# Kernel optimization log

Hardware: AMD Instinct MI355X
Metric: run time of the kernel (lower is better)

The kernel has to match this reference:

```python
import jax, jax.numpy as jnp
import numpy as np

# config (matches init_kwargs)
D_MODEL = 2048
EXPAND = 2
HEADDIM = 64
D_STATE = 128
D_CONV = 4
NGROUPS = 1  # reference implemented for ngroups == 1
CHUNK = 256
EPS = 1e-5
D_INNER = EXPAND * D_MODEL            # 4096
NHEADS = D_INNER // HEADDIM           # 64
CONV_DIM = D_INNER + 2 * NGROUPS * D_STATE   # 4352
D_IN_PROJ = 2 * D_INNER + 2 * NGROUPS * D_STATE + NHEADS  # 8512
BATCH, SEQLEN = 2, 2048


def segsum(a):
    # a: [..., q] log-decays -> [..., q, q] with entry (i,j) = sum_{j<k<=i} a_k, -inf above diag
    T = a.shape[-1]
    cs = jnp.cumsum(a, axis=-1)
    d = cs[..., :, None] - cs[..., None, :]
    mask = jnp.tril(jnp.ones((T, T), dtype=bool))
    return jnp.where(mask, d, -jnp.inf)


def setup_inputs() -> dict:
    key = jax.random.key(0)
    ks = jax.random.split(key, 8)
    u = jax.random.normal(ks[0], (BATCH, SEQLEN, D_MODEL), jnp.float32)
    in_proj_w = jax.random.normal(ks[1], (D_IN_PROJ, D_MODEL), jnp.float32) / np.sqrt(D_MODEL).astype(np.float32)
    conv_w = jax.random.normal(ks[2], (CONV_DIM, D_CONV), jnp.float32) / np.sqrt(D_CONV).astype(np.float32)
    conv_b = jnp.zeros((CONV_DIM,), jnp.float32)
    # dt_bias init as in module: inv-softplus of dt ~ LogUniform(1e-3, 1e-1)
    dt0 = jnp.exp(jax.random.uniform(ks[3], (NHEADS,), jnp.float32)
                  * (np.log(0.1) - np.log(0.001)) + np.log(0.001))
    dt0 = jnp.clip(dt0, 1e-4, None)
    dt_bias = dt0 + jnp.log(-jnp.expm1(-dt0))
    A_log = jnp.log(jax.random.uniform(ks[4], (NHEADS,), jnp.float32, minval=1.0, maxval=16.0))
    D = jnp.ones((NHEADS,), jnp.float32)
    norm_w = jnp.ones((D_INNER,), jnp.float32)
    out_proj_w = jax.random.normal(ks[5], (D_MODEL, D_INNER), jnp.float32) / np.sqrt(D_INNER).astype(np.float32)
    return dict(u=u, in_proj_w=in_proj_w, conv_w=conv_w, conv_b=conv_b,
                dt_bias=dt_bias, A_log=A_log, D=D, norm_w=norm_w, out_proj_w=out_proj_w)


def reference(u, in_proj_w, conv_w, conv_b, dt_bias, A_log, D, norm_w, out_proj_w):
    b, l, _ = u.shape
    # in_proj -> [z | xBC | dt]  (d_mlp == 0 for this config)
    zxbcdt = jnp.einsum('bld,ed->ble', u, in_proj_w)
    z = zxbcdt[..., :D_INNER]
    xBC = zxbcdt[..., D_INNER:D_INNER + CONV_DIM]
    dt = zxbcdt[..., D_INNER + CONV_DIM:]                      # [b,l,h]

    # causal depthwise conv1d + SiLU (kernel D_CONV, left padding)
    xp = jnp.pad(xBC, ((0, 0), (D_CONV - 1, 0), (0, 0)))
    conv = conv_b
    for k in range(D_CONV):
        conv = conv + xp[:, k:k + l, :] * conv_w[:, k]
    xBC = jax.nn.silu(conv)

    x = xBC[..., :D_INNER]
    Bm = xBC[..., D_INNER:D_INNER + D_STATE]                   # [b,l,n] (ngroups=1)
    Cm = xBC[..., D_INNER + D_STATE:]                          # [b,l,n]

    dtv = jax.nn.softplus(dt + dt_bias)                        # [b,l,h]
    A = -jnp.exp(A_log)                                        # [h]
    xh = x.reshape(b, l, NHEADS, HEADDIM)

    # ---- chunked SSD scan (mamba_chunk_scan_combined) ----
    c = l // CHUNK
    xc = (xh * dtv[..., None]).reshape(b, c, CHUNK, NHEADS, HEADDIM)   # dt-scaled inputs
    Ac = (dtv * A).reshape(b, c, CHUNK, NHEADS).transpose(0, 3, 1, 2)  # [b,h,c,q] log decays
    Bc = Bm.reshape(b, c, CHUNK, D_STATE)
    Cc = Cm.reshape(b, c, CHUNK, D_STATE)

    Acum = jnp.cumsum(Ac, axis=-1)                              # [b,h,c,q]
    Lmat = jnp.exp(segsum(Ac))                                  # [b,h,c,q,q] causal decay matrix
    # intra-chunk (diagonal block) contribution
    Y_diag = jnp.einsum('bcqn,bcsn,bhcqs,bcshp->bcqhp', Cc, Bc, Lmat, xc)
    # per-chunk end states
    decay_states = jnp.exp(Acum[..., -1:] - Acum)               # [b,h,c,q]
    states = jnp.einsum('bcsn,bhcs,bcshp->bchpn', Bc, decay_states, xc)
    chunk_decay = jnp.exp(Acum[..., -1])                        # [b,h,c]

    def step(S, inp):
        st, dec = inp                                           # [b,h,p,n], [b,h]
        return dec[..., None, None] * S + st, S

    S0 = jnp.zeros((b, NHEADS, HEADDIM, D_STATE), xc.dtype)
    _, prev = jax.lax.scan(step, S0,
                           (states.transpose(1, 0, 2, 3, 4), chunk_decay.transpose(2, 0, 1)))
    prev = prev.transpose(1, 0, 2, 3, 4)                        # [b,c,h,p,n] states entering each chunk
    # inter-chunk contribution
    Y_off = jnp.einsum('bcqn,bchpn,bhcq->bcqhp', Cc, prev, jnp.exp(Acum))

    y = (Y_diag + Y_off).reshape(b, l, NHEADS, HEADDIM)
    y = y + D[:, None] * xh                                     # skip connection D*x
    # gate (applied inside kernel via z=...), then gated RMSNorm (z-less here), then out_proj
    y = y.reshape(b, l, D_INNER) * jax.nn.silu(z)
    y = y * jax.lax.rsqrt(jnp.mean(jnp.square(y), axis=-1, keepdims=True) + EPS) * norm_w
    return jnp.einsum('bld,ed->ble', y, out_proj_w)
```

## Files before the change

### kernel.cpp

```cpp
#include <hip/hip_runtime.h>
#include <cstddef>
#include <cstdint>

#define BATCH   2
#define SEQLEN  2048
#define DMODEL  2048
#define DINNER  4096
#define NHEADS  64
#define HEADDIM 64
#define DSTATE  128
#define DCONV   4
#define CHUNKSZ 256
#define NCHUNK  (SEQLEN / CHUNKSZ)
#define CONVDIM (DINNER + 2 * DSTATE)
#define DINPROJ (2 * DINNER + 2 * DSTATE + NHEADS)
#define BL      (BATCH * SEQLEN)
#define EPSV    1e-5f

typedef __attribute__((ext_vector_type(8))) short short8v;
typedef __attribute__((ext_vector_type(4))) float floatx4;

__device__ __forceinline__ float sigmoidf_(float x) { return 1.f / (1.f + expf(-x)); }

__device__ __forceinline__ unsigned short f2bf(float x) {
  uint32_t u = __float_as_uint(x);
  uint32_t r = (u + 0x7FFFu + ((u >> 16) & 1u)) >> 16;
  return (unsigned short)r;
}
__device__ __forceinline__ float bf2f(unsigned short h) {
  return __uint_as_float(((uint32_t)h) << 16);
}

__device__ __forceinline__ void gload16(const void* g, void* l) {
  __builtin_amdgcn_global_load_lds((const __attribute__((address_space(1))) void*)g,
                                   (__attribute__((address_space(3))) void*)l, 16, 0, 0);
}

__global__ __launch_bounds__(256) void split4_kernel(const float* __restrict__ x,
                                                     unsigned short* __restrict__ hi,
                                                     unsigned short* __restrict__ lo,
                                                     int n4) {
  int i = blockIdx.x * 256 + threadIdx.x;
  if (i >= n4) return;
  float4 v = ((const float4*)x)[i];
  ushort4 hv, lv;
  hv.x = f2bf(v.x); lv.x = f2bf(v.x - bf2f(hv.x));
  hv.y = f2bf(v.y); lv.y = f2bf(v.y - bf2f(hv.y));
  hv.z = f2bf(v.z); lv.z = f2bf(v.z - bf2f(hv.z));
  hv.w = f2bf(v.w); lv.w = f2bf(v.w - bf2f(hv.w));
  ((ushort4*)hi)[i] = hv;
  ((ushort4*)lo)[i] = lv;
}

template <int EPI>
__global__ __launch_bounds__(256) void gemm3bf(const unsigned short* __restrict__ Ah,
                                               const unsigned short* __restrict__ Al, int lda,
                                               const unsigned short* __restrict__ Bh,
                                               const unsigned short* __restrict__ Bl, int ldb,
                                               int M, int N, int K,
                                               float* __restrict__ o0, float* __restrict__ o1,
                                               float* __restrict__ o2) {
  __shared__ __align__(16) unsigned short lds[4][4][128][8];
  const int tid = threadIdx.x;
  const int lane = tid & 63;
  const int w = tid >> 6, wm = w >> 1, wn = w & 1;
  const int bm = blockIdx.y * 128, bn = blockIdx.x * 128;
  const int r16 = lane & 15, kg = lane >> 4;
  floatx4 acc[4][4] = {};

  for (int k0 = 0; k0 < K; k0 += 32) {
#pragma unroll
    for (int arr = 0; arr < 4; ++arr) {
      const unsigned short* src = (arr == 0) ? Ah : (arr == 1) ? Al : (arr == 2) ? Bh : Bl;
      const int ld = (arr < 2) ? lda : ldb;
#pragma unroll
      for (int t = 0; t < 2; ++t) {
        int ubase = t * 256 + w * 64;
        int u = ubase + lane;
        int g = u >> 7, m = u & 127;
        int row;
        if (arr < 2) row = bm + m;
        else { row = bn + m; if (row >= N) row = N - 1; }
        const unsigned short* gp = src + (size_t)row * ld + k0 + g * 8;
        gload16(gp, (void*)(&lds[arr][0][0][0] + (size_t)ubase * 8));
      }
    }
    __syncthreads();

    short8v bhf[4], blf[4];
#pragma unroll
    for (int j = 0; j < 4; ++j) {
      int n_in = wn * 64 + j * 16 + r16;
      bhf[j] = *(const short8v*)&lds[2][kg][n_in][0];
      blf[j] = *(const short8v*)&lds[3][kg][n_in][0];
    }
#pragma unroll
    for (int i = 0; i < 4; ++i) {
      int m_in = wm * 64 + i * 16 + r16;
      short8v ah = *(const short8v*)&lds[0][kg][m_in][0];
      short8v al = *(const short8v*)&lds[1][kg][m_in][0];
#pragma unroll
      for (int j = 0; j < 4; ++j) {
        acc[i][j] = __builtin_amdgcn_mfma_f32_16x16x32_bf16(ah, bhf[j], acc[i][j], 0, 0, 0);
        acc[i][j] = __builtin_amdgcn_mfma_f32_16x16x32_bf16(ah, blf[j], acc[i][j], 0, 0, 0);
        acc[i][j] = __builtin_amdgcn_mfma_f32_16x16x32_bf16(al, bhf[j], acc[i][j], 0, 0, 0);
      }
    }
    __syncthreads();
  }

#pragma unroll
  for (int i = 0; i < 4; ++i) {
#pragma unroll
    for (int j = 0; j < 4; ++j) {
      int n = bn + wn * 64 + j * 16 + r16;
#pragma unroll
      for (int r = 0; r < 4; ++r) {
        int m = bm + wm * 64 + i * 16 + kg * 4 + r;
        float v = acc[i][j][r];
        if (EPI == 0) {
          o0[(size_t)m * N + n] = v;
        } else {
          if (n < DINNER) o0[(size_t)m * DINNER + n] = v;
          else if (n < DINNER + CONVDIM) o1[(size_t)m * CONVDIM + (n - DINNER)] = v;
          else if (n < DINPROJ) o2[(size_t)m * NHEADS + (n - DINNER - CONVDIM)] = v;
        }
      }
    }
  }
}

__global__ __launch_bounds__(256) void conv_silu_split(const float* __restrict__ xbc,
                                                       const float* __restrict__ cw,
                                                       const float* __restrict__ cb,
                                                       float* __restrict__ xb,
                                                       float* __restrict__ bbuf,
                                                       float* __restrict__ cbuf) {
  int idx = blockIdx.x * 256 + threadIdx.x;
  if (idx >= BL * CONVDIM) return;
  int ch = idx % CONVDIM;
  int bl = idx / CONVDIM;
  int l = bl & (SEQLEN - 1);
  int b = bl / SEQLEN;
  float acc = cb[ch];
#pragma unroll
  for (int k = 0; k < DCONV; ++k) {
    int ls = l - (DCONV - 1) + k;
    if (ls >= 0)
      acc = fmaf(xbc[((size_t)(b * SEQLEN + ls)) * CONVDIM + ch], cw[ch * DCONV + k], acc);
  }
  float s = acc * sigmoidf_(acc);
  if (ch < DINNER)
    xb[(size_t)bl * DINNER + ch] = s;
  else if (ch < DINNER + DSTATE)
    bbuf[(size_t)bl * DSTATE + (ch - DINNER)] = s;
  else
    cbuf[(size_t)bl * DSTATE + (ch - DINNER - DSTATE)] = s;
}

__global__ __launch_bounds__(256) void dt_kernel(const float* __restrict__ dtraw,
                                                 const float* __restrict__ dt_bias,
                                                 const float* __restrict__ A_log,
                                                 float* __restrict__ dtv,
                                                 float* dAb) {
  int idx = blockIdx.x * 256 + threadIdx.x;
  if (idx >= BL * NHEADS) return;
  int h = idx & (NHEADS - 1);
  float dtr = dtraw[idx] + dt_bias[h];
  float v = (dtr > 20.f) ? dtr : log1pf(expf(dtr));
  dtv[idx] = v;
  dAb[idx] = -expf(A_log[h]) * v;
}

__global__ __launch_bounds__(256) void cumsum_kernel(const float* __restrict__ dAb,
                                                     float* __restrict__ acum,
                                                     float* __restrict__ cdec) {
  const int bch = blockIdx.x;
  const int h = bch & (NHEADS - 1);
  const int bc = bch >> 6;
  const int b = bc >> 3, c = bc & (NCHUNK - 1);
  const int s = threadIdx.x;
  __shared__ float buf[CHUNKSZ];
  buf[s] = dAb[((size_t)(b * SEQLEN) + c * CHUNKSZ + s) * NHEADS + h];
  __syncthreads();
  for (int off = 1; off < CHUNKSZ; off <<= 1) {
    float t = (s >= off) ? buf[s - off] : 0.f;
    __syncthreads();
    buf[s] += t;
    __syncthreads();
  }
  float r = buf[s];
  acum[(size_t)bch * CHUNKSZ + s] = r;
  if (s == CHUNKSZ - 1) cdec[bch] = expf(r);
}

__global__ __launch_bounds__(256) void states_kernel(const float* __restrict__ xb,
                                                     const float* __restrict__ bbuf,
                                                     const float* __restrict__ dtv,
                                                     const float* __restrict__ acum,
                                                     float* __restrict__ states) {
  const int bch = blockIdx.x;
  const int h = bch & (NHEADS - 1);
  const int bc = bch >> 6;
  const int b = bc >> 3, c = bc & (NCHUNK - 1);
  const float* ac = acum + (size_t)bch * CHUNKSZ;
  const float clast = ac[CHUNKSZ - 1];
  __shared__ float xs[32][65];
  __shared__ float bs[32][129];
  __shared__ float wsh[32];
  const int tid = threadIdx.x;
  const int tp = tid >> 4, tn = tid & 15;
  float acc[4][8] = {};
  for (int s0 = 0; s0 < CHUNKSZ; s0 += 32) {
    if (tid < 32) {
      int s = s0 + tid;
      wsh[tid] = expf(clast - ac[s]) *
                 dtv[((size_t)(b * SEQLEN) + c * CHUNKSZ + s) * NHEADS + h];
    }
    __syncthreads();
    for (int e = tid; e < 32 * 64; e += 256) {
      int s = e >> 6, pp = e & 63;
      xs[s][pp] = xb[((size_t)(b * SEQLEN) + c * CHUNKSZ + s0 + s) * DINNER + h * HEADDIM + pp] * wsh[s];
    }
    for (int e = tid; e < 32 * 128; e += 256) {
      int s = e >> 7, n = e & 127;
      bs[s][n] = bbuf[((size_t)(b * SEQLEN) + c * CHUNKSZ + s0 + s) * DSTATE + n];
    }
    __syncthreads();
#pragma unroll 8
    for (int s = 0; s < 32; ++s) {
      float a[4], bv[8];
#pragma unroll
      for (int i = 0; i < 4; ++i) a[i] = xs[s][tp * 4 + i];
#pragma unroll
      for (int j = 0; j < 8; ++j) bv[j] = bs[s][tn * 8 + j];
#pragma unroll
      for (int i = 0; i < 4; ++i)
#pragma unroll
        for (int j = 0; j < 8; ++j)
          acc[i][j] = fmaf(a[i], bv[j], acc[i][j]);
    }
    __syncthreads();
  }
#pragma unroll
  for (int i = 0; i < 4; ++i)
#pragma unroll
    for (int j = 0; j < 8; ++j)
      states[((size_t)bch * HEADDIM + tp * 4 + i) * DSTATE + tn * 8 + j] = acc[i][j];
}

__global__ __launch_bounds__(256) void scan_kernel(float* __restrict__ states,
                                                   const float* __restrict__ cdec) {
  int idx = blockIdx.x * 256 + threadIdx.x;
  const int pn = idx & (HEADDIM * DSTATE - 1);
  const int bh = idx >> 13;
  const int h = bh & (NHEADS - 1), b = bh >> 6;
  float S = 0.f;
  for (int c = 0; c < NCHUNK; ++c) {
    int bch = (b * NCHUNK + c) * NHEADS + h;
    size_t off = (size_t)bch * (HEADDIM * DSTATE) + pn;
    float st = states[off];
    states[off] = S;
    S = fmaf(cdec[bch], S, st);
  }
}

__global__ __launch_bounds__(256) void cb_kernel(const float* __restrict__ cbuf,
                                                 const float* __restrict__ bbuf,
                                                 float* __restrict__ g0) {
  const int qb = blockIdx.x >> 2, sb = blockIdx.x & 3;
  if (sb > qb) return;
  const int bc = blockIdx.y;
  const int tid = threadIdx.x;
  __shared__ float As[16][65];
  __shared__ float Bs[16][65];
  const int lr = tid >> 2, lk = (tid & 3) << 2;
  const int tx = tid & 15, ty = tid >> 4;
  float acc[4][4] = {};
  const float* Arow = cbuf + ((size_t)bc * CHUNKSZ + qb * 64) * DSTATE;
  const float* Brow = bbuf + ((size_t)bc * CHUNKSZ + sb * 64) * DSTATE;
  for (int k0 = 0; k0 < DSTATE; k0 += 16) {
    float4 av = *(const float4*)(Arow + (size_t)lr * DSTATE + k0 + lk);
    float4 bv = *(const float4*)(Brow + (size_t)lr * DSTATE + k0 + lk);
    As[lk + 0][lr] = av.x; As[lk + 1][lr] = av.y; As[lk + 2][lr] = av.z; As[lk + 3][lr] = av.w;
    Bs[lk + 0][lr] = bv.x; Bs[lk + 1][lr] = bv.y; Bs[lk + 2][lr] = bv.z; Bs[lk + 3][lr] = bv.w;
    __syncthreads();
#pragma unroll
    for (int kk = 0; kk < 16; ++kk) {
      float a[4], bv2[4];
#pragma unroll
      for (int i = 0; i < 4; ++i) a[i] = As[kk][ty * 4 + i];
#pragma unroll
      for (int j = 0; j < 4; ++j) bv2[j] = Bs[kk][tx * 4 + j];
#pragma unroll
      for (int i = 0; i < 4; ++i)
#pragma unroll
        for (int j = 0; j < 4; ++j)
          acc[i][j] = fmaf(a[i], bv2[j], acc[i][j]);
    }
    __syncthreads();
  }
#pragma unroll
  for (int i = 0; i < 4; ++i)
#pragma unroll
    for (int j = 0; j < 4; ++j)
      g0[((size_t)bc * CHUNKSZ + qb * 64 + ty * 4 + i) * CHUNKSZ + sb * 64 + tx * 4 + j] = acc[i][j];
}

__global__ __launch_bounds__(256) void y_kernel(const float* __restrict__ xb,
                                                const float* __restrict__ cbuf,
                                                const float* __restrict__ g0,
                                                const float* __restrict__ acum,
                                                const float* __restrict__ dtv,
                                                const float* __restrict__ prevb,
                                                const float* __restrict__ Dvec,
                                                float* __restrict__ yb) {
  const int qb = blockIdx.x & 3;
  const int h = (blockIdx.x >> 2) & (NHEADS - 1);
  const int bc = blockIdx.x >> 8;
  const int b = bc >> 3, c = bc & (NCHUNK - 1);
  const int tid = threadIdx.x;
  const int tq = tid >> 4, tp = tid & 15;
  const float* ac = acum + ((size_t)bc * NHEADS + h) * CHUNKSZ;
  __shared__ float gs[64][33];
  __shared__ float xs[32][65];
  __shared__ float ps[64][33];
  const int qbase = qb * 64;
  float acc[4][4] = {};
  for (int s0 = 0; s0 < qbase + 64; s0 += 32) {
    for (int e = tid; e < 64 * 32; e += 256) {
      int q = e >> 5, s = e & 31;
      int gq = qbase + q, gsd = s0 + s;
      float v = 0.f;
      if (gsd <= gq) {
        float lw = expf(ac[gq] - ac[gsd]);
        float dv = dtv[((size_t)(b * SEQLEN) + c * CHUNKSZ + gsd) * NHEADS + h];
        v = g0[((size_t)bc * CHUNKSZ + gq) * CHUNKSZ + gsd] * lw * dv;
      }
      gs[q][s] = v;
    }
    for (int e = tid; e < 32 * 64; e += 256) {
      int s = e >> 6, pp = e & 63;
      xs[s][pp] = xb[((size_t)(b * SEQLEN) + c * CHUNKSZ + s0 + s) * DINNER + h * HEADDIM + pp];
    }
    __syncthreads();
#pragma unroll 8
    for (int s = 0; s < 32; ++s) {
      float a[4], xv[4];
#pragma unroll
      for (int i = 0; i < 4; ++i) a[i] = gs[tq * 4 + i][s];
#pragma unroll
      for (int j = 0; j < 4; ++j) xv[j] = xs[s][tp * 4 + j];
#pragma unroll
      for (int i = 0; i < 4; ++i)
#pragma unroll
        for (int j = 0; j < 4; ++j)
          acc[i][j] = fmaf(a[i], xv[j], acc[i][j]);
    }
    __syncthreads();
  }
  float acc2[4][4] = {};
  for (int n0 = 0; n0 < DSTATE; n0 += 32) {
    for (int e = tid; e < 64 * 32; e += 256) {
      int q = e >> 5, n = e & 31;
      gs[q][n] = cbuf[((size_t)(b * SEQLEN) + c * CHUNKSZ + qbase + q) * DSTATE + n0 + n];
    }
    for (int e = tid; e < 64 * 32; e += 256) {
      int pp = e >> 5, n = e & 31;
      ps[pp][n] = prevb[(((size_t)bc * NHEADS + h) * HEADDIM + pp) * DSTATE + n0 + n];
    }
    __syncthreads();
#pragma unroll 8
    for (int n = 0; n < 32; ++n) {
      float a[4], pv[4];
#pragma unroll
      for (int i = 0; i < 4; ++i) a[i] = gs[tq * 4 + i][n];
#pragma unroll
      for (int j = 0; j < 4; ++j) pv[j] = ps[tp * 4 + j][n];
#pragma unroll
      for (int i = 0; i < 4; ++i)
#pragma unroll
        for (int j = 0; j < 4; ++j)
          acc2[i][j] = fmaf(a[i], pv[j], acc2[i][j]);
    }
    __syncthreads();
  }
  const float dh = Dvec[h];
#pragma unroll
  for (int i = 0; i < 4; ++i) {
    int q = qbase + tq * 4 + i;
    float eaq = expf(ac[q]);
    size_t row = ((size_t)(b * SEQLEN) + c * CHUNKSZ + q) * DINNER + h * HEADDIM;
#pragma unroll
    for (int j = 0; j < 4; ++j) {
      int pp = tp * 4 + j;
      float xv = xb[row + pp];
      yb[row + pp] = acc[i][j] + eaq * acc2[i][j] + dh * xv;
    }
  }
}

__global__ __launch_bounds__(256) void norm_kernel(float* yb,
                                                   const float* __restrict__ zbuf,
                                                   const float* __restrict__ nw) {
  const int bl = blockIdx.x;
  float* y = yb + (size_t)bl * DINNER;
  const float* z = zbuf + (size_t)bl * DINNER;
  float vals[16];
  float ss = 0.f;
  int j = 0;
  for (int i = threadIdx.x; i < DINNER; i += 256, ++j) {
    float zz = z[i];
    float g = y[i] * zz * sigmoidf_(zz);
    vals[j] = g;
    ss = fmaf(g, g, ss);
  }
  for (int off = 32; off > 0; off >>= 1) ss += __shfl_down(ss, off, 64);
  __shared__ float red[4];
  if ((threadIdx.x & 63) == 0) red[threadIdx.x >> 6] = ss;
  __syncthreads();
  float tot = red[0] + red[1] + red[2] + red[3];
  float scale = rsqrtf(tot * (1.f / DINNER) + EPSV);
  unsigned short* yh = (unsigned short*)y;
  unsigned short* yl = yh + DINNER;
  j = 0;
  for (int i = threadIdx.x; i < DINNER; i += 256, ++j) {
    float v = vals[j] * scale * nw[i];
    unsigned short h = f2bf(v);
    yh[i] = h;
    yl[i] = f2bf(v - bf2f(h));
  }
}

extern "C" void kernel_launch(void* const* d_in, const int* in_sizes, int n_in,
                              void* d_out, int out_size, void* d_ws, size_t ws_size,
                              hipStream_t stream) {
  const float* u        = (const float*)d_in[0];
  const float* Wp       = (const float*)d_in[1];
  const float* conv_w   = (const float*)d_in[2];
  const float* conv_b   = (const float*)d_in[3];
  const float* dt_bias  = (const float*)d_in[4];
  const float* A_log    = (const float*)d_in[5];
  const float* Dvec     = (const float*)d_in[6];
  const float* norm_w   = (const float*)d_in[7];
  const float* Wo       = (const float*)d_in[8];
  float* out = (float*)d_out;

  char* p = (char*)d_ws;
  auto alloc = [&](size_t nfloats) {
    float* r = (float*)p;
    p += nfloats * sizeof(float);
    return r;
  };
  float* zbuf   = alloc((size_t)BL * DINNER);
  float* xbc    = alloc((size_t)BL * CONVDIM);
  float* dtraw  = alloc((size_t)BL * NHEADS);
  float* xb     = alloc((size_t)BL * DINNER);
  float* bbuf   = alloc((size_t)BL * DSTATE);
  float* cbuf   = alloc((size_t)BL * DSTATE);
  float* dtvb   = alloc((size_t)BL * NHEADS);
  float* acum   = alloc((size_t)BATCH * NCHUNK * NHEADS * CHUNKSZ);
  float* cdec   = alloc((size_t)BATCH * NCHUNK * NHEADS);
  float* dAb    = dtraw;
  float* states = out;
  float* g0     = xbc + (size_t)BL * DINNER;
  float* yb     = xbc;
  unsigned short* u_hi  = (unsigned short*)d_out;
  unsigned short* u_lo  = u_hi + (size_t)BL * DMODEL;
  unsigned short* wp_hi = (unsigned short*)xb;
  unsigned short* wp_lo = wp_hi + (size_t)DINPROJ * DMODEL;
  unsigned short* wo_hi = (unsigned short*)zbuf;
  unsigned short* wo_lo = wo_hi + (size_t)DMODEL * DINNER;
  unsigned short* yo_hi = (unsigned short*)xbc;
  unsigned short* yo_lo = yo_hi + DINNER;

  split4_kernel<<<(BL * DMODEL / 4 + 255) / 256, 256, 0, stream>>>(u, u_hi, u_lo, BL * DMODEL / 4);
  split4_kernel<<<(DINPROJ * DMODEL / 4 + 255) / 256, 256, 0, stream>>>(Wp, wp_hi, wp_lo,
                                                                        DINPROJ * DMODEL / 4);
  gemm3bf<1><<<dim3((DINPROJ + 127) / 128, BL / 128), 256, 0, stream>>>(
      u_hi, u_lo, DMODEL, wp_hi, wp_lo, DMODEL, BL, DINPROJ, DMODEL, zbuf, xbc, dtraw);
  conv_silu_split<<<(BL * CONVDIM + 255) / 256, 256, 0, stream>>>(xbc, conv_w, conv_b, xb, bbuf, cbuf);
  dt_kernel<<<(BL * NHEADS + 255) / 256, 256, 0, stream>>>(dtraw, dt_bias, A_log, dtvb, dAb);
  cumsum_kernel<<<BATCH * NCHUNK * NHEADS, CHUNKSZ, 0, stream>>>(dAb, acum, cdec);
  states_kernel<<<BATCH * NCHUNK * NHEADS, 256, 0, stream>>>(xb, bbuf, dtvb, acum, states);
  scan_kernel<<<(BATCH * NHEADS * HEADDIM * DSTATE) / 256, 256, 0, stream>>>(states, cdec);
  cb_kernel<<<dim3(16, BATCH * NCHUNK), 256, 0, stream>>>(cbuf, bbuf, g0);
  y_kernel<<<BATCH * NCHUNK * NHEADS * 4, 256, 0, stream>>>(xb, cbuf, g0, acum, dtvb, states, Dvec, yb);
  norm_kernel<<<BL, 256, 0, stream>>>(yb, zbuf, norm_w);
  split4_kernel<<<(DMODEL * DINNER / 4 + 255) / 256, 256, 0, stream>>>(Wo, wo_hi, wo_lo,
                                                                      DMODEL * DINNER / 4);
  gemm3bf<0><<<dim3(DMODEL / 128, BL / 128), 256, 0, stream>>>(
      yo_hi, yo_lo, 2 * DINNER, wo_hi, wo_lo, DINNER, BL, DMODEL, DINNER, out, nullptr, nullptr);
}
```

Before: 1.735 ms.

## Double-buffer LDS in split-bf16 GEMM, add grouped XCD-aware tile swizzle

Gives the 3xbf16 GEMM two LDS buffers, so the next K-slice's global-to-LDS loads are issued before the current slice's MFMAs. This cuts one barrier per iteration. The launch becomes a 1D grid remapped through an XCD-round-robin swizzle and grouped-M ordering to improve L2 reuse of the operand tiles. Output stores become nontemporal. LDS use doubles to 64KB per block, which may lower occupancy, and nontemporal stores could hurt the consumer kernels that reread these outputs.

```diff
diff --git a/kernel.cpp b/kernel.cpp
--- a/kernel.cpp
+++ b/kernel.cpp
@@ -60,45 +60,69 @@
                                                int M, int N, int K,
                                                float* __restrict__ o0, float* __restrict__ o1,
                                                float* __restrict__ o2) {
-  __shared__ __align__(16) unsigned short lds[4][4][128][8];
+  __shared__ __align__(16) unsigned short lds[2][4][4][128][8];
   const int tid = threadIdx.x;
   const int lane = tid & 63;
   const int w = tid >> 6, wm = w >> 1, wn = w & 1;
-  const int bm = blockIdx.y * 128, bn = blockIdx.x * 128;
   const int r16 = lane & 15, kg = lane >> 4;
+
+  const int nbm = M >> 7;
+  const int nbn = (N + 127) >> 7;
+  const int nblk = nbm * nbn;
+  int wgid = blockIdx.x;
+  if ((nblk & 7) == 0) {
+    int q = nblk >> 3;
+    wgid = (wgid & 7) * q + (wgid >> 3);
+  }
+  const int GM = 8;
+  const int per_group = GM * nbn;
+  const int group = wgid / per_group;
+  const int gm0 = group * GM;
+  int rows = nbm - gm0; if (rows > GM) rows = GM;
+  const int rem = wgid - group * per_group;
+  const int pm = gm0 + rem % rows;
+  const int pn = rem / rows;
+  const int bm = pm * 128, bn = pn * 128;
+
   floatx4 acc[4][4] = {};
 
-  for (int k0 = 0; k0 < K; k0 += 32) {
+  auto stage = [&](int buf, int k0) {
 #pragma unroll
     for (int arr = 0; arr < 4; ++arr) {
       const unsigned short* src = (arr == 0) ? Ah : (arr == 1) ? Al : (arr == 2) ? Bh : Bl;
       const int ld = (arr < 2) ? lda : ldb;
 #pragma unroll
-      for (int t = 0; t < 2; ++t) {
-        int ubase = t * 256 + w * 64;
+      for (int t2 = 0; t2 < 2; ++t2) {
+        int ubase = t2 * 256 + w * 64;
         int u = ubase + lane;
         int g = u >> 7, m = u & 127;
         int row;
         if (arr < 2) row = bm + m;
         else { row = bn + m; if (row >= N) row = N - 1; }
         const unsigned short* gp = src + (size_t)row * ld + k0 + g * 8;
-        gload16(gp, (void*)(&lds[arr][0][0][0] + (size_t)ubase * 8));
+        gload16(gp, (void*)(&lds[buf][arr][0][0][0] + (size_t)ubase * 8));
       }
     }
-    __syncthreads();
-
+  };
+
+  const int nt = K >> 5;
+  stage(0, 0);
+  int cur = 0;
+  for (int t = 0; t < nt; ++t) {
+    __syncthreads();
+    if (t + 1 < nt) stage(cur ^ 1, (t + 1) << 5);
     short8v bhf[4], blf[4];
 #pragma unroll
     for (int j = 0; j < 4; ++j) {
       int n_in = wn * 64 + j * 16 + r16;
-      bhf[j] = *(const short8v*)&lds[2][kg][n_in][0];
-      blf[j] = *(const short8v*)&lds[3][kg][n_in][0];
+      bhf[j] = *(const short8v*)&lds[cur][2][kg][n_in][0];
+      blf[j] = *(const short8v*)&lds[cur][3][kg][n_in][0];
     }
 #pragma unroll
     for (int i = 0; i < 4; ++i) {
       int m_in = wm * 64 + i * 16 + r16;
-      short8v ah = *(const short8v*)&lds[0][kg][m_in][0];
-      short8v al = *(const short8v*)&lds[1][kg][m_in][0];
+      short8v ah = *(const short8v*)&lds[cur][0][kg][m_in][0];
+      short8v al = *(const short8v*)&lds[cur][1][kg][m_in][0];
 #pragma unroll
       for (int j = 0; j < 4; ++j) {
         acc[i][j] = __builtin_amdgcn_mfma_f32_16x16x32_bf16(ah, bhf[j], acc[i][j], 0, 0, 0);
@@ -106,7 +130,7 @@
         acc[i][j] = __builtin_amdgcn_mfma_f32_16x16x32_bf16(al, bhf[j], acc[i][j], 0, 0, 0);
       }
     }
-    __syncthreads();
+    cur ^= 1;
   }
 
 #pragma unroll
@@ -119,11 +143,14 @@
         int m = bm + wm * 64 + i * 16 + kg * 4 + r;
         float v = acc[i][j][r];
         if (EPI == 0) {
-          o0[(size_t)m * N + n] = v;
+          __builtin_nontemporal_store(v, &o0[(size_t)m * N + n]);
         } else {
-          if (n < DINNER) o0[(size_t)m * DINNER + n] = v;
-          else if (n < DINNER + CONVDIM) o1[(size_t)m * CONVDIM + (n - DINNER)] = v;
-          else if (n < DINPROJ) o2[(size_t)m * NHEADS + (n - DINNER - CONVDIM)] = v;
+          if (n < DINNER)
+            __builtin_nontemporal_store(v, &o0[(size_t)m * DINNER + n]);
+          else if (n < DINNER + CONVDIM)
+            __builtin_nontemporal_store(v, &o1[(size_t)m * CONVDIM + (n - DINNER)]);
+          else if (n < DINPROJ)
+            __builtin_nontemporal_store(v, &o2[(size_t)m * NHEADS + (n - DINNER - CONVDIM)]);
         }
       }
     }
@@ -477,7 +504,7 @@
   split4_kernel<<<(BL * DMODEL / 4 + 255) / 256, 256, 0, stream>>>(u, u_hi, u_lo, BL * DMODEL / 4);
   split4_kernel<<<(DINPROJ * DMODEL / 4 + 255) / 256, 256, 0, stream>>>(Wp, wp_hi, wp_lo,
                                                                         DINPROJ * DMODEL / 4);
-  gemm3bf<1><<<dim3((DINPROJ + 127) / 128, BL / 128), 256, 0, stream>>>(
+  gemm3bf<1><<<((DINPROJ + 127) / 128) * (BL / 128), 256, 0, stream>>>(
       u_hi, u_lo, DMODEL, wp_hi, wp_lo, DMODEL, BL, DINPROJ, DMODEL, zbuf, xbc, dtraw);
   conv_silu_split<<<(BL * CONVDIM + 255) / 256, 256, 0, stream>>>(xbc, conv_w, conv_b, xb, bbuf, cbuf);
   dt_kernel<<<(BL * NHEADS + 255) / 256, 256, 0, stream>>>(dtraw, dt_bias, A_log, dtvb, dAb);
@@ -489,6 +516,6 @@
   norm_kernel<<<BL, 256, 0, stream>>>(yb, zbuf, norm_w);
   split4_kernel<<<(DMODEL * DINNER / 4 + 255) / 256, 256, 0, stream>>>(Wo, wo_hi, wo_lo,
                                                                       DMODEL * DINNER / 4);
-  gemm3bf<0><<<dim3(DMODEL / 128, BL / 128), 256, 0, stream>>>(
+  gemm3bf<0><<<(DMODEL / 128) * (BL / 128), 256, 0, stream>>>(
       yo_hi, yo_lo, 2 * DINNER, wo_hi, wo_lo, DINNER, BL, DMODEL, DINNER, out, nullptr, nullptr);
 }
```

Measured after the change: 1.678 ms. -3.3%, faster.
